# Performance work log

Hardware: AMD Instinct MI355X
Metric: run time of the kernel (lower is better)

## Reference

```python
import jax, jax.numpy as jnp
import numpy as np

EPS = 1e-7
BLOCK = 64  # block_size from init_kwargs


def project(x):
    norm = jnp.clip(jnp.linalg.norm(x, axis=-1, keepdims=True), EPS)
    return jnp.where(norm >= 1.0, x / norm * (1.0 - EPS), x)


def mobius_add(x, y, c):
    x2 = jnp.sum(x * x, -1, keepdims=True)
    y2 = jnp.sum(y * y, -1, keepdims=True)
    xy = jnp.sum(x * y, -1, keepdims=True)
    num = (1 + 2 * c * xy + c * y2) * x + (1 - c * x2) * y
    den = 1 + 2 * c * xy + c * c * x2 * y2
    return project(num / jnp.clip(den, EPS))


def logmap0(y, c):
    sqrt_c = jnp.clip(jnp.sqrt(c), EPS)
    yn = jnp.linalg.norm(y, axis=-1, keepdims=True)
    mag = jnp.arctanh(jnp.minimum(yn, 1.0 - EPS)) / sqrt_c
    return jnp.where(yn < EPS, jnp.zeros_like(y), mag * (y / jnp.clip(yn, EPS)))


def expmap0(v, c):
    sqrt_c = jnp.clip(jnp.sqrt(c), EPS)
    vn = jnp.linalg.norm(v, axis=-1, keepdims=True)
    mag = jnp.tanh(sqrt_c * jnp.clip(vn, EPS)) / sqrt_c
    return project(jnp.where(vn < EPS, jnp.zeros_like(v), mag * (v / jnp.clip(vn, EPS))))


def pdist(x, y, c):
    # x: [B,H,S,1,D], y: [B,H,1,S,D], c: [1,H,1,1,1] -> [B,H,S,S]
    sqrt_c = jnp.clip(jnp.sqrt(c), EPS)
    add_norm = jnp.linalg.norm(mobius_add(-x, y, c), axis=-1)
    sc = jnp.squeeze(sqrt_c, -1)
    arg = jnp.minimum(sc * add_norm, 1.0 - EPS)
    return 2.0 * jnp.arctanh(arg) / sc


def layernorm(x, scale, bias, eps=1e-6):
    mu = jnp.mean(x, -1, keepdims=True)
    var = jnp.mean(jnp.square(x - mu), -1, keepdims=True)
    return (x - mu) * jax.lax.rsqrt(var + eps) * scale + bias


def precompute_freqs_cis(dim, end, theta=10000.0):
    f = 1.0 / theta ** (jnp.arange(0, dim, 2, dtype=jnp.float32) / dim)
    return jnp.exp(1j * jnp.outer(jnp.arange(end), f))


def rope(x, fc):
    # split-half rotary, as in WubuBlock.apply_rotary_emb
    xr, xi = jnp.split(x, 2, -1)
    xc = jax.lax.complex(xr, xi) * fc.reshape(1, 1, fc.shape[0], fc.shape[1])
    return jnp.concatenate([xc.real, xc.imag], -1)


def setup_inputs() -> dict:
    key = jax.random.key(0)
    ks = jax.random.split(key, 8)
    B, N, D, H = 1, 1024, 512, 8
    w = lambda k, shape, s=0.02: jax.random.normal(k, shape, jnp.float32) * s
    return {
        'x': w(ks[0], (B, N, D), 0.02),  # points well inside the Poincare ball
        'c_global': jax.random.uniform(ks[1], (B, 1), jnp.float32, 0.5, 1.5),
        'W_qkv': w(ks[2], (D, 3 * D)), 'b_qkv': jnp.zeros((3 * D,), jnp.float32),
        'W_out': w(ks[3], (D, D)), 'b_out': jnp.zeros((D,), jnp.float32),
        'ln1_scale': jnp.ones((D,), jnp.float32), 'ln1_bias': jnp.zeros((D,), jnp.float32),
        'ln2_scale': jnp.ones((D,), jnp.float32), 'ln2_bias': jnp.zeros((D,), jnp.float32),
        'W_ff1': w(ks[4], (D, 4 * D)), 'b_ff1': jnp.zeros((4 * D,), jnp.float32),
        'W_ff2': w(ks[5], (4 * D, D)), 'b_ff2': jnp.zeros((D,), jnp.float32),
        'c_per_head_logits': jnp.zeros((H,), jnp.float32),
        'geo_scale': jnp.ones((1, H, 1, 1), jnp.float32),
        'start_pos': 0,
    }


def reference(x, c_global, W_qkv, b_qkv, W_out, b_out, ln1_scale, ln1_bias,
              ln2_scale, ln2_bias, W_ff1, b_ff1, W_ff2, b_ff2,
              c_per_head_logits, geo_scale, start_pos):
    B, N, D = x.shape
    H = c_per_head_logits.shape[0]
    hd = D // H
    S = BLOCK
    nb = N // S
    Be = B * nb
    xb = x.reshape(Be, S, D)
    c_b = jnp.repeat(c_global, nb, axis=0).reshape(Be, 1, 1)

    # tangent-space layernorm (norm1) then logmap to tangent for QKV proj
    xn = expmap0(layernorm(logmap0(xb, c_b), ln1_scale, ln1_bias), c_b)
    xt = logmap0(xn, c_b)
    qkv = (xt @ W_qkv + b_qkv).reshape(Be, S, 3, H, hd).transpose(2, 0, 3, 1, 4)
    q, k, v = qkv[0], qkv[1], qkv[2]  # [Be,H,S,hd]

    fc = precompute_freqs_cis(hd, S)
    q = rope(q, fc)
    k = rope(k, fc)

    c_h = jax.nn.softplus(c_per_head_logits).reshape(1, H, 1, 1)
    qh = expmap0(q, c_h)
    kh = expmap0(k, c_h)

    # full pairwise hyperbolic distance: [Be,H,S,S]
    d = pdist(qh[:, :, :, None, :], kh[:, :, None, :, :], c_h[:, :, None, :, :])
    attn = jax.nn.softmax(-geo_scale * d, axis=-1)
    ao = jnp.einsum('bhqk,bhkd->bhqd', attn, v)
    ao = ao.transpose(0, 2, 1, 3).reshape(Be, S, D)

    ah = expmap0(ao @ W_out + b_out, c_b)
    xa = mobius_add(xb, ah, c_b)  # hyperbolic residual

    # hyperbolic FFN with tangent-space norm (norm2)
    xn2 = expmap0(layernorm(logmap0(xa, c_b), ln2_scale, ln2_bias), c_b)
    t = logmap0(xn2, c_b)
    fh = expmap0(jax.nn.gelu(t @ W_ff1 + b_ff1) @ W_ff2 + b_ff2, c_b)
    out = mobius_add(xa, fh, c_b)
    return out.reshape(B, N, D)
```

## Files before the change

### kernel.cpp

```cpp
#include <hip/hip_runtime.h>
#include <math.h>

#define DEV __device__ __forceinline__
typedef _Float16 h16;
typedef __attribute__((ext_vector_type(8))) _Float16 h8v;
typedef __attribute__((ext_vector_type(4))) _Float16 h4v;
typedef __attribute__((ext_vector_type(4))) float f4v;

constexpr int NTOK = 1024;
constexpr int D    = 512;
constexpr int H    = 8;
constexpr int NB   = 16;
constexpr double EPSd = 1e-7;

DEV double wave_sum(double v) {
#pragma unroll
  for (int m = 32; m; m >>= 1) v += __shfl_xor(v, m, 64);
  return v;
}

__global__ void k_prep(const float* __restrict__ Wqkv, const float* __restrict__ Wout,
                       const float* __restrict__ Wff1, const float* __restrict__ Wff2,
                       const float* __restrict__ x, const float* __restrict__ cg,
                       const float* __restrict__ s1, const float* __restrict__ b1,
                       h16* __restrict__ qT, h16* __restrict__ oT,
                       h16* __restrict__ f1T, h16* __restrict__ f2T,
                       h16* __restrict__ xt) {
  __shared__ float t[32][33];
  const int bid = blockIdx.x;
  if (bid < 3072) {
    const float* src; h16* dh; int K, N, bx, by;
    if (bid < 768)       { src = Wqkv; dh = qT;  K = 512;  N = 1536; bx = bid % 48;          by = bid / 48; }
    else if (bid < 1024) { src = Wout; dh = oT;  K = 512;  N = 512;  bx = (bid - 768) % 16;  by = (bid - 768) / 16; }
    else if (bid < 2048) { src = Wff1; dh = f1T; K = 512;  N = 2048; bx = (bid - 1024) % 64; by = (bid - 1024) / 64; }
    else                 { src = Wff2; dh = f2T; K = 2048; N = 512;  bx = (bid - 2048) % 16; by = (bid - 2048) / 16; }
    const int n0 = bx * 32, k0 = by * 32;
    const int tx = threadIdx.x & 31, ty = threadIdx.x >> 5;
    for (int i = ty; i < 32; i += 8) t[i][tx] = src[(size_t)(k0 + i) * N + n0 + tx];
    __syncthreads();
    for (int i = ty; i < 32; i += 8)
      dh[(size_t)(n0 + i) * K + k0 + tx] = (h16)t[tx][i];
    return;
  }
  const int wid = threadIdx.x >> 6, lane = threadIdx.x & 63;
  const int tok = (bid - 3072) * 4 + wid;
  const float4* xr = (const float4*)(x + (size_t)tok * D);
  float4 xv0 = xr[lane], xv1 = xr[lane + 64];
  double sv = 0.0, svv = 0.0;
  {
    const float e[8] = {xv0.x, xv0.y, xv0.z, xv0.w, xv1.x, xv1.y, xv1.z, xv1.w};
#pragma unroll
    for (int j = 0; j < 8; ++j) { double d = e[j]; sv += d; svv += d * d; }
  }
  sv = wave_sum(sv); svv = wave_sum(svv);
  double c = (double)cg[0];
  double sc = sqrt(c); if (sc < EPSd) sc = EPSd;
  double yn = sqrt(svv);
  double arg0 = yn; if (arg0 > 1.0 - EPSd) arg0 = 1.0 - EPSd;
  double f = (yn < EPSd) ? 0.0 : atanh(arg0) / sc / fmax(yn, EPSd);
  double mu = f * sv / D;
  double var = f * f * svv / D - mu * mu;
  double rs = 1.0 / sqrt(var + 1e-6);
  const float4* s1r = (const float4*)s1;
  const float4* b1r = (const float4*)b1;
  float4 sA = s1r[lane], sB = s1r[lane + 64];
  float4 bA = b1r[lane], bB = b1r[lane + 64];
  double w[8]; double sww = 0.0;
  {
    const float e[8]  = {xv0.x, xv0.y, xv0.z, xv0.w, xv1.x, xv1.y, xv1.z, xv1.w};
    const float se[8] = {sA.x, sA.y, sA.z, sA.w, sB.x, sB.y, sB.z, sB.w};
    const float be[8] = {bA.x, bA.y, bA.z, bA.w, bB.x, bB.y, bB.z, bB.w};
#pragma unroll
    for (int j = 0; j < 8; ++j) {
      w[j] = (f * (double)e[j] - mu) * rs * (double)se[j] + (double)be[j];
      sww += w[j] * w[j];
    }
  }
  sww = wave_sum(sww);
  double vn = sqrt(sww);
  double F = 0.0;
  if (vn >= EPSd) {
    double mag_e = tanh(sc * fmax(vn, EPSd)) / sc;
    F = atanh(fmin(mag_e, 1.0 - EPSd)) / (sc * vn);
  }
  h16* dst = xt + (size_t)tok * D;
#pragma unroll
  for (int half = 0; half < 2; ++half) {
    h4v o;
#pragma unroll
    for (int e = 0; e < 4; ++e) o[e] = (h16)(float)(F * w[half * 4 + e]);
    *(h4v*)(dst + 4 * (lane + 64 * half)) = o;
  }
}

DEV void stage_tile(const h16* __restrict__ gbase, int rowstride, h16* lds,
                    int wid, int lane) {
#pragma unroll
  for (int j = 0; j < 2; ++j) {
    const int rbase = wid * 16 + j * 8;
    const int grow = rbase + (lane >> 3);
    const int gch = (lane & 7) ^ (lane >> 3);
    const h16* gp = gbase + (size_t)grow * rowstride + gch * 8;
    __builtin_amdgcn_global_load_lds(
        (const __attribute__((address_space(1))) void*)gp,
        (__attribute__((address_space(3))) void*)(lds + rbase * 64), 16, 0, 0);
  }
}
DEV h8v read_frag(const h16* lds, int row, int c) {
  const int p = c ^ (row & 7);
  return *(const h8v*)(lds + row * 64 + p * 8);
}

template <int GELU, int OHALF, int SPLITK>
__global__ __launch_bounds__(256) void k_mm(
    const h16* __restrict__ A, const h16* __restrict__ B,
    const float* __restrict__ bias, float* __restrict__ Cf, h16* __restrict__ Ch,
    int M, int N, int K) {
  __shared__ __align__(16) h16 As[2][64 * 64];
  __shared__ __align__(16) h16 Bs[2][64 * 64];
  const int tid = threadIdx.x;
  const int lane = tid & 63, wid = tid >> 6;
  const int wr = (wid >> 1) * 32, wc = (wid & 1) * 32;
  const int lr = lane & 15, lg = lane >> 4;
  const size_t r0 = (size_t)blockIdx.y * 64, c0 = (size_t)blockIdx.x * 64;
  const int kz = SPLITK ? blockIdx.z : 0;
  const int Keff = SPLITK ? (K >> 1) : K;
  const f4v z = {0.f, 0.f, 0.f, 0.f};
  f4v acc[2][2]; acc[0][0] = z; acc[0][1] = z; acc[1][0] = z; acc[1][1] = z;
  const h16* Abase = A + r0 * K + (size_t)kz * Keff;
  const h16* Bbase = B + c0 * K + (size_t)kz * Keff;
  const int NT = Keff >> 6;
  stage_tile(Abase, K, As[0], wid, lane);
  stage_tile(Bbase, K, Bs[0], wid, lane);
  int cur = 0;
  for (int t = 0; t < NT; ++t) {
    const int nxt = cur ^ 1;
    if (t + 1 < NT) {
      stage_tile(Abase + (t + 1) * 64, K, As[nxt], wid, lane);
      stage_tile(Bbase + (t + 1) * 64, K, Bs[nxt], wid, lane);
      asm volatile("s_waitcnt vmcnt(4)" ::: "memory");
    } else {
      asm volatile("s_waitcnt vmcnt(0)" ::: "memory");
    }
    asm volatile("s_barrier" ::: "memory");
    const h16* Ac = As[cur];
    const h16* Bc = Bs[cur];
#pragma unroll
    for (int ks = 0; ks < 2; ++ks) {
      const int c = ks * 4 + lg;
      h8v a0 = read_frag(Ac, wr + lr, c);
      h8v a1 = read_frag(Ac, wr + 16 + lr, c);
      h8v b0 = read_frag(Bc, wc + lr, c);
      h8v b1 = read_frag(Bc, wc + 16 + lr, c);
      acc[0][0] = __builtin_amdgcn_mfma_f32_16x16x32_f16(a0, b0, acc[0][0], 0, 0, 0);
      acc[0][1] = __builtin_amdgcn_mfma_f32_16x16x32_f16(a0, b1, acc[0][1], 0, 0, 0);
      acc[1][0] = __builtin_amdgcn_mfma_f32_16x16x32_f16(a1, b0, acc[1][0], 0, 0, 0);
      acc[1][1] = __builtin_amdgcn_mfma_f32_16x16x32_f16(a1, b1, acc[1][1], 0, 0, 0);
    }
    asm volatile("s_barrier" ::: "memory");
    cur = nxt;
  }
  float* Cfo = Cf + (size_t)kz * M * N;
#pragma unroll
  for (int m = 0; m < 2; ++m)
#pragma unroll
    for (int n = 0; n < 2; ++n) {
      const size_t row = r0 + wr + m * 16 + lg * 4;
      const size_t col = c0 + wc + n * 16 + lr;
      const float bv = (SPLITK && kz) ? 0.f : bias[col];
#pragma unroll
      for (int e = 0; e < 4; ++e) {
        float v = acc[m][n][e] + bv;
        if (GELU) {
          float x3 = v * v * v;
          v = 0.5f * v * (1.0f + tanhf(0.7978845608028654f * (v + 0.044715f * x3)));
        }
        if (OHALF) Ch[(row + e) * N + col] = (h16)v;
        else       Cfo[(row + e) * N + col] = v;
      }
    }
}

__global__ __launch_bounds__(256) void k_attn(
    const h16* __restrict__ qkv, const float* __restrict__ chl,
    const float* __restrict__ geo, h16* __restrict__ ao) {
  __shared__ __align__(16) float Qs[32][68];
  __shared__ __align__(16) float Kt[64][68];
  __shared__ __align__(16) float Vs[64][68];
  __shared__ float q2s[32], k2s[64], fqv[32], fkv[64];
  const int bid = blockIdx.x;
  const int be = bid >> 4, h = (bid >> 1) & 7, q0 = (bid & 1) * 32;
  const int tid = threadIdx.x;
  const double chd = log1p(exp((double)chl[h]));
  const float ch = (float)chd;
  float sc = (float)sqrt(chd); if (sc < 1e-7f) sc = 1e-7f;
  for (int l = tid; l < 64 * 32; l += 256) {
    int s = l >> 5, j = l & 31;
    const h16* base = qkv + (size_t)(be * 64 + s) * 1536 + h * 64;
    float ka = (float)base[512 + j], kb = (float)base[512 + j + 32];
    float fj = expf((float)j * -0.2878231366242557f);
    float st, ct; sincosf((float)s * fj, &st, &ct);
    Kt[j][s]      = ka * ct - kb * st;
    Kt[j + 32][s] = ka * st + kb * ct;
    Vs[s][j]      = (float)base[1024 + j];
    Vs[s][j + 32] = (float)base[1024 + j + 32];
  }
  for (int l = tid; l < 32 * 32; l += 256) {
    int s = l >> 5, j = l & 31;
    const h16* base = qkv + (size_t)(be * 64 + q0 + s) * 1536 + h * 64;
    float qa = (float)base[j], qb = (float)base[j + 32];
    float fj = expf((float)j * -0.2878231366242557f);
    float st, ct; sincosf((float)(q0 + s) * fj, &st, &ct);
    Qs[s][j]      = qa * ct - qb * st;
    Qs[s][j + 32] = qa * st + qb * ct;
  }
  __syncthreads();
  if (tid < 64) {
    float a = 0.f;
    for (int d2 = 0; d2 < 64; ++d2) { float v = Kt[d2][tid]; a += v * v; }
    float n = sqrtf(a);
    float m = tanhf(sc * fmaxf(n, 1e-7f)) / sc;
    float f = (n < 1e-7f) ? 0.f : m / fmaxf(n, 1e-7f);
    if (m >= 1.f) f *= (1.f - 1e-7f) / m;
    float fn = f * n;
    fkv[tid] = f; k2s[tid] = fn * fn;
  } else if (tid < 96) {
    int i = tid - 64;
    float a = 0.f;
    for (int d2 = 0; d2 < 64; ++d2) { float v = Qs[i][d2]; a += v * v; }
    float n = sqrtf(a);
    float m = tanhf(sc * fmaxf(n, 1e-7f)) / sc;
    float f = (n < 1e-7f) ? 0.f : m / fmaxf(n, 1e-7f);
    if (m >= 1.f) f *= (1.f - 1e-7f) / m;
    float fn = f * n;
    fqv[i] = f; q2s[i] = fn * fn;
  }
  __syncthreads();
  const int i = tid >> 3, g = tid & 7;
  float gacc[8];
#pragma unroll
  for (int jj = 0; jj < 8; ++jj) gacc[jj] = 0.f;
  for (int d2 = 0; d2 < 64; ++d2) {
    float qv = Qs[i][d2];
    const float4* kp = (const float4*)&Kt[d2][g * 8];
    float4 k0 = kp[0], k1 = kp[1];
    gacc[0] += qv * k0.x; gacc[1] += qv * k0.y; gacc[2] += qv * k0.z; gacc[3] += qv * k0.w;
    gacc[4] += qv * k1.x; gacc[5] += qv * k1.y; gacc[6] += qv * k1.z; gacc[7] += qv * k1.w;
  }
  const float gs = geo[h];
  const float q2 = q2s[i], fqi = fqv[i];
  float lg[8];
  float mx = -1e30f;
#pragma unroll
  for (int jj = 0; jj < 8; ++jj) {
    float gq = fqi * fkv[g * 8 + jj] * gacc[jj];
    float k2 = k2s[g * 8 + jj];
    float A  = 1.f - 2.f * ch * gq + ch * k2;
    float Bv = 1.f - ch * q2;
    float n2 = fmaxf(A * A * q2 - 2.f * A * Bv * gq + Bv * Bv * k2, 0.f);
    float den = fmaxf(1.f - 2.f * ch * gq + ch * ch * q2 * k2, 1e-7f);
    float r = fminf(sqrtf(n2) / den, 1.f - 1e-7f);
    float arg = fminf(sc * r, 1.f - 1e-7f);
    float l = -gs * (2.f * atanhf(arg) / sc);
    lg[jj] = l; mx = fmaxf(mx, l);
  }
  mx = fmaxf(mx, __shfl_xor(mx, 1, 64));
  mx = fmaxf(mx, __shfl_xor(mx, 2, 64));
  mx = fmaxf(mx, __shfl_xor(mx, 4, 64));
  float pv[8]; float sum = 0.f;
#pragma unroll
  for (int jj = 0; jj < 8; ++jj) { pv[jj] = expf(lg[jj] - mx); sum += pv[jj]; }
  sum += __shfl_xor(sum, 1, 64);
  sum += __shfl_xor(sum, 2, 64);
  sum += __shfl_xor(sum, 4, 64);
  float inv = 1.0f / sum;
#pragma unroll
  for (int jj = 0; jj < 8; ++jj) Qs[i][g * 8 + jj] = pv[jj] * inv;
  float oacc[8];
#pragma unroll
  for (int dd = 0; dd < 8; ++dd) oacc[dd] = 0.f;
  for (int jv = 0; jv < 64; ++jv) {
    float p = Qs[i][jv];
    const float4* vp = (const float4*)&Vs[jv][g * 8];
    float4 v0 = vp[0], v1 = vp[1];
    oacc[0] += p * v0.x; oacc[1] += p * v0.y; oacc[2] += p * v0.z; oacc[3] += p * v0.w;
    oacc[4] += p * v1.x; oacc[5] += p * v1.y; oacc[6] += p * v1.z; oacc[7] += p * v1.w;
  }
#pragma unroll
  for (int dd = 0; dd < 8; ++dd)
    ao[(size_t)(be * 64 + q0 + i) * D + h * 64 + g * 8 + dd] = (h16)oacc[dd];
}

__global__ void k_resid(const float* __restrict__ x, const float* __restrict__ proj,
                        const float* __restrict__ cg, const float* __restrict__ s2,
                        const float* __restrict__ b2, float* __restrict__ xa,
                        h16* __restrict__ t2) {
  const int wid = threadIdx.x >> 6, lane = threadIdx.x & 63;
  const int tok = blockIdx.x * 4 + wid;
  const float4* xr  = (const float4*)(x + (size_t)tok * D);
  const float4* p0r = (const float4*)(proj + (size_t)tok * D);
  const float4* p1r = (const float4*)(proj + (size_t)NTOK * D + (size_t)tok * D);
  float4 xv0 = xr[lane], xv1 = xr[lane + 64];
  float4 pa0 = p0r[lane], pa1 = p0r[lane + 64];
  float4 pb0 = p1r[lane], pb1 = p1r[lane + 64];
  float pe[8], xe[8];
  xe[0]=xv0.x; xe[1]=xv0.y; xe[2]=xv0.z; xe[3]=xv0.w; xe[4]=xv1.x; xe[5]=xv1.y; xe[6]=xv1.z; xe[7]=xv1.w;
  pe[0]=pa0.x+pb0.x; pe[1]=pa0.y+pb0.y; pe[2]=pa0.z+pb0.z; pe[3]=pa0.w+pb0.w;
  pe[4]=pa1.x+pb1.x; pe[5]=pa1.y+pb1.y; pe[6]=pa1.z+pb1.z; pe[7]=pa1.w+pb1.w;
  double sx = 0, sp = 0, xx = 0, pp = 0, xp = 0;
#pragma unroll
  for (int j = 0; j < 8; ++j) {
    double dx = xe[j], dp = pe[j];
    sx += dx; sp += dp; xx += dx * dx; pp += dp * dp; xp += dx * dp;
  }
  sx = wave_sum(sx); sp = wave_sum(sp); xx = wave_sum(xx);
  pp = wave_sum(pp); xp = wave_sum(xp);
  double c = (double)cg[0];
  double sc = sqrt(c); if (sc < EPSd) sc = EPSd;
  double pn = sqrt(pp);
  double me = tanh(sc * fmax(pn, EPSd)) / sc;
  double fs = (pn < EPSd) ? 0.0 : me / fmax(pn, EPSd);
  if (me >= 1.0) fs *= (1.0 - EPSd) / me;
  double y2 = fs * fs * pp, xy = fs * xp;
  double a = 1.0 + 2.0 * c * xy + c * y2;
  double b = 1.0 - c * xx;
  double den = 1.0 + 2.0 * c * xy + c * c * xx * y2;
  if (den < EPSd) den = EPSd;
  double zn = sqrt(fmax(a * a * xx + 2.0 * a * b * xy + b * b * y2, 0.0)) / den;
  double zs = 1.0 / den;
  if (zn >= 1.0) zs *= (1.0 - EPSd) / zn;
  double xan = (zn >= 1.0) ? (1.0 - EPSd) : zn;
  double A0 = zs * a, B0 = zs * b * fs;
  double xav[8];
#pragma unroll
  for (int j = 0; j < 8; ++j) xav[j] = A0 * (double)xe[j] + B0 * (double)pe[j];
  {
    float4 o0 = {(float)xav[0], (float)xav[1], (float)xav[2], (float)xav[3]};
    float4 o1 = {(float)xav[4], (float)xav[5], (float)xav[6], (float)xav[7]};
    float4* xw = (float4*)(xa + (size_t)tok * D);
    xw[lane] = o0; xw[lane + 64] = o1;
  }
  double sxa  = A0 * sx + B0 * sp;
  double sxa2 = A0 * A0 * xx + 2.0 * A0 * B0 * xp + B0 * B0 * pp;
  double fl = 0.0;
  if (xan >= EPSd) fl = atanh(fmin(xan, 1.0 - EPSd)) / (sc * fmax(xan, EPSd));
  double mu = fl * sxa / D;
  double var = fl * fl * sxa2 / D - mu * mu;
  double rs = 1.0 / sqrt(var + 1e-6);
  const float4* s2r = (const float4*)s2;
  const float4* b2r = (const float4*)b2;
  float4 sA = s2r[lane], sB = s2r[lane + 64];
  float4 bA = b2r[lane], bB = b2r[lane + 64];
  const float se[8] = {sA.x, sA.y, sA.z, sA.w, sB.x, sB.y, sB.z, sB.w};
  const float be[8] = {bA.x, bA.y, bA.z, bA.w, bB.x, bB.y, bB.z, bB.w};
  double w[8]; double sww = 0.0;
#pragma unroll
  for (int j = 0; j < 8; ++j) {
    w[j] = (fl * xav[j] - mu) * rs * (double)se[j] + (double)be[j];
    sww += w[j] * w[j];
  }
  sww = wave_sum(sww);
  double vn = sqrt(sww);
  double F = 0.0;
  if (vn >= EPSd) {
    double mag_e = tanh(sc * fmax(vn, EPSd)) / sc;
    F = atanh(fmin(mag_e, 1.0 - EPSd)) / (sc * vn);
  }
  h16* dst = t2 + (size_t)tok * D;
#pragma unroll
  for (int half = 0; half < 2; ++half) {
    h4v o;
#pragma unroll
    for (int e = 0; e < 4; ++e) o[e] = (h16)(float)(F * w[half * 4 + e]);
    *(h4v*)(dst + 4 * (lane + 64 * half)) = o;
  }
}

__global__ void k_final(const float* __restrict__ xa, const float* __restrict__ f2,
                        const float* __restrict__ cg, float* __restrict__ out) {
  const int wid = threadIdx.x >> 6, lane = threadIdx.x & 63;
  const int tok = blockIdx.x * 4 + wid;
  const float4* ar  = (const float4*)(xa + (size_t)tok * D);
  const float4* f0r = (const float4*)(f2 + (size_t)tok * D);
  const float4* f1r = (const float4*)(f2 + (size_t)NTOK * D + (size_t)tok * D);
  float4 xv0 = ar[lane], xv1 = ar[lane + 64];
  float4 pa0 = f0r[lane], pa1 = f0r[lane + 64];
  float4 pb0 = f1r[lane], pb1 = f1r[lane + 64];
  float pe[8], xe[8];
  xe[0]=xv0.x; xe[1]=xv0.y; xe[2]=xv0.z; xe[3]=xv0.w; xe[4]=xv1.x; xe[5]=xv1.y; xe[6]=xv1.z; xe[7]=xv1.w;
  pe[0]=pa0.x+pb0.x; pe[1]=pa0.y+pb0.y; pe[2]=pa0.z+pb0.z; pe[3]=pa0.w+pb0.w;
  pe[4]=pa1.x+pb1.x; pe[5]=pa1.y+pb1.y; pe[6]=pa1.z+pb1.z; pe[7]=pa1.w+pb1.w;
  double xx = 0, pp = 0, xp = 0;
#pragma unroll
  for (int j = 0; j < 8; ++j) {
    double dx = xe[j], dp = pe[j];
    xx += dx * dx; pp += dp * dp; xp += dx * dp;
  }
  xx = wave_sum(xx); pp = wave_sum(pp); xp = wave_sum(xp);
  double c = (double)cg[0];
  double sc = sqrt(c); if (sc < EPSd) sc = EPSd;
  double pn = sqrt(pp);
  double me = tanh(sc * fmax(pn, EPSd)) / sc;
  double fs = (pn < EPSd) ? 0.0 : me / fmax(pn, EPSd);
  if (me >= 1.0) fs *= (1.0 - EPSd) / me;
  double y2 = fs * fs * pp, xy = fs * xp;
  double a = 1.0 + 2.0 * c * xy + c * y2;
  double b = 1.0 - c * xx;
  double den = 1.0 + 2.0 * c * xy + c * c * xx * y2;
  if (den < EPSd) den = EPSd;
  double zn = sqrt(fmax(a * a * xx + 2.0 * a * b * xy + b * b * y2, 0.0)) / den;
  double zs = 1.0 / den;
  if (zn >= 1.0) zs *= (1.0 - EPSd) / zn;
  double A0 = zs * a, B0 = zs * b * fs;
  float4 o0, o1;
  o0.x = (float)(A0 * xe[0] + B0 * pe[0]); o0.y = (float)(A0 * xe[1] + B0 * pe[1]);
  o0.z = (float)(A0 * xe[2] + B0 * pe[2]); o0.w = (float)(A0 * xe[3] + B0 * pe[3]);
  o1.x = (float)(A0 * xe[4] + B0 * pe[4]); o1.y = (float)(A0 * xe[5] + B0 * pe[5]);
  o1.z = (float)(A0 * xe[6] + B0 * pe[6]); o1.w = (float)(A0 * xe[7] + B0 * pe[7]);
  float4* ow = (float4*)(out + (size_t)tok * D);
  ow[lane] = o0; ow[lane + 64] = o1;
}

extern "C" void kernel_launch(void* const* d_in, const int* in_sizes, int n_in,
                              void* d_out, int out_size, void* d_ws, size_t ws_size,
                              hipStream_t stream) {
  (void)in_sizes; (void)n_in; (void)out_size; (void)ws_size;
  const float* x    = (const float*)d_in[0];
  const float* cg   = (const float*)d_in[1];
  const float* Wqkv = (const float*)d_in[2];
  const float* bqkv = (const float*)d_in[3];
  const float* Wout = (const float*)d_in[4];
  const float* bout = (const float*)d_in[5];
  const float* s1   = (const float*)d_in[6];
  const float* b1   = (const float*)d_in[7];
  const float* s2   = (const float*)d_in[8];
  const float* b2   = (const float*)d_in[9];
  const float* Wff1 = (const float*)d_in[10];
  const float* bff1 = (const float*)d_in[11];
  const float* Wff2 = (const float*)d_in[12];
  const float* bff2 = (const float*)d_in[13];
  const float* chl  = (const float*)d_in[14];
  const float* geo  = (const float*)d_in[15];
  float* out = (float*)d_out;

  char* base = (char*)d_ws;
  const size_t MB = 1024 * 1024;
  h16*   WqkvT = (h16*)(base + 0);
  h16*   WoutT = (h16*)(base + (3*MB)/2);
  h16*   Wff1T = (h16*)(base + 2*MB);
  h16*   Wff2T = (h16*)(base + 4*MB);
  h16*   xt    = (h16*)(base + 6*MB);
  h16*   qkv   = (h16*)(base + 7*MB);
  h16*   ao    = (h16*)(base + 10*MB);
  float* proj  = (float*)(base + 11*MB);
  float* xa    = (float*)(base + 7*MB);
  h16*   t2    = (h16*)(base + 6*MB);
  h16*   h1    = (h16*)(base + 11*MB);
  float* f2    = (float*)(base + 0);

  k_prep<<<3072 + NTOK / 4, 256, 0, stream>>>(Wqkv, Wout, Wff1, Wff2, x, cg, s1, b1,
                                              WqkvT, WoutT, Wff1T, Wff2T, xt);
  k_mm<0, 1, 0><<<dim3(1536 / 64, NTOK / 64), 256, 0, stream>>>(
      xt, WqkvT, bqkv, nullptr, qkv, NTOK, 1536, 512);
  k_attn<<<NB * H * 2, 256, 0, stream>>>(qkv, chl, geo, ao);
  k_mm<0, 0, 1><<<dim3(512 / 64, NTOK / 64, 2), 256, 0, stream>>>(
      ao, WoutT, bout, proj, nullptr, NTOK, 512, 512);
  k_resid<<<NTOK / 4, 256, 0, stream>>>(x, proj, cg, s2, b2, xa, t2);
  k_mm<1, 1, 0><<<dim3(2048 / 64, NTOK / 64), 256, 0, stream>>>(
      t2, Wff1T, bff1, nullptr, h1, NTOK, 2048, 512);
  k_mm<0, 0, 1><<<dim3(512 / 64, NTOK / 64, 2), 256, 0, stream>>>(
      h1, Wff2T, bff2, f2, nullptr, NTOK, 512, 2048);
  k_final<<<NTOK / 4, 256, 0, stream>>>(xa, f2, cg, out);
}
```

Before: 74.89 us.

## Triple-buffer GEMM tiles and vectorize attention Q/K/V staging with fused norms

The GEMM kernel moves from a double-buffered to a triple-buffered LDS pipeline, prefetching two K-tiles ahead with adjusted vmcnt waits so global loads overlap more MFMA work. The attention kernel loads Q, K and V with 16-byte half8 vector loads, one thread per 8-element chunk, and computes the squared norms during RoPE using the rotation-invariance of the norm. This removes the serial 64-step LDS norm loops, and the output store becomes a single 16-byte write. The costs are 50% more LDS per GEMM block, which can lower occupancy, and more live registers in the staging loop.

```diff
diff --git a/kernel.cpp b/kernel.cpp
--- a/kernel.cpp
+++ b/kernel.cpp
@@ -116,8 +116,8 @@
     const h16* __restrict__ A, const h16* __restrict__ B,
     const float* __restrict__ bias, float* __restrict__ Cf, h16* __restrict__ Ch,
     int M, int N, int K) {
-  __shared__ __align__(16) h16 As[2][64 * 64];
-  __shared__ __align__(16) h16 Bs[2][64 * 64];
+  __shared__ __align__(16) h16 As[3][64 * 64];
+  __shared__ __align__(16) h16 Bs[3][64 * 64];
   const int tid = threadIdx.x;
   const int lane = tid & 63, wid = tid >> 6;
   const int wr = (wid >> 1) * 32, wc = (wid & 1) * 32;
@@ -132,16 +132,20 @@
   const int NT = Keff >> 6;
   stage_tile(Abase, K, As[0], wid, lane);
   stage_tile(Bbase, K, Bs[0], wid, lane);
+  stage_tile(Abase + 64, K, As[1], wid, lane);
+  stage_tile(Bbase + 64, K, Bs[1], wid, lane);
   int cur = 0;
   for (int t = 0; t < NT; ++t) {
-    const int nxt = cur ^ 1;
-    if (t + 1 < NT) {
-      stage_tile(Abase + (t + 1) * 64, K, As[nxt], wid, lane);
-      stage_tile(Bbase + (t + 1) * 64, K, Bs[nxt], wid, lane);
-      asm volatile("s_waitcnt vmcnt(4)" ::: "memory");
-    } else {
-      asm volatile("s_waitcnt vmcnt(0)" ::: "memory");
+    const int pre = (cur == 2) ? 0 : cur + 1;
+    const int pre2 = (pre == 2) ? 0 : pre + 1;
+    if (t + 2 < NT) {
+      stage_tile(Abase + (t + 2) * 64, K, As[pre2], wid, lane);
+      stage_tile(Bbase + (t + 2) * 64, K, Bs[pre2], wid, lane);
     }
+    const int rem = NT - 1 - t;
+    if (rem >= 2)      asm volatile("s_waitcnt vmcnt(8)" ::: "memory");
+    else if (rem == 1) asm volatile("s_waitcnt vmcnt(4)" ::: "memory");
+    else               asm volatile("s_waitcnt vmcnt(0)" ::: "memory");
     asm volatile("s_barrier" ::: "memory");
     const h16* Ac = As[cur];
     const h16* Bc = Bs[cur];
@@ -158,7 +162,7 @@
       acc[1][1] = __builtin_amdgcn_mfma_f32_16x16x32_f16(a1, b1, acc[1][1], 0, 0, 0);
     }
     asm volatile("s_barrier" ::: "memory");
-    cur = nxt;
+    cur = pre;
   }
   float* Cfo = Cf + (size_t)kz * M * N;
 #pragma unroll
@@ -187,6 +191,7 @@
   __shared__ __align__(16) float Qs[32][68];
   __shared__ __align__(16) float Kt[64][68];
   __shared__ __align__(16) float Vs[64][68];
+  __shared__ float q2raw[32], k2raw[64];
   __shared__ float q2s[32], k2s[64], fqv[32], fkv[64];
   const int bid = blockIdx.x;
   const int be = bid >> 4, h = (bid >> 1) & 7, q0 = (bid & 1) * 32;
@@ -194,31 +199,61 @@
   const double chd = log1p(exp((double)chl[h]));
   const float ch = (float)chd;
   float sc = (float)sqrt(chd); if (sc < 1e-7f) sc = 1e-7f;
-  for (int l = tid; l < 64 * 32; l += 256) {
-    int s = l >> 5, j = l & 31;
+  {
+    const int s = tid >> 2, jc = (tid & 3) * 8;
     const h16* base = qkv + (size_t)(be * 64 + s) * 1536 + h * 64;
-    float ka = (float)base[512 + j], kb = (float)base[512 + j + 32];
-    float fj = expf((float)j * -0.2878231366242557f);
-    float st, ct; sincosf((float)s * fj, &st, &ct);
-    Kt[j][s]      = ka * ct - kb * st;
-    Kt[j + 32][s] = ka * st + kb * ct;
-    Vs[s][j]      = (float)base[1024 + j];
-    Vs[s][j + 32] = (float)base[1024 + j + 32];
-  }
-  for (int l = tid; l < 32 * 32; l += 256) {
-    int s = l >> 5, j = l & 31;
+    h8v klo = *(const h8v*)(base + 512 + jc);
+    h8v khi = *(const h8v*)(base + 512 + jc + 32);
+    h8v vlo = *(const h8v*)(base + 1024 + jc);
+    h8v vhi = *(const h8v*)(base + 1024 + jc + 32);
+    float racc = 0.f;
+#pragma unroll
+    for (int j = 0; j < 8; ++j) {
+      float ka = (float)klo[j], kb = (float)khi[j];
+      racc += ka * ka + kb * kb;
+      float fj = expf((float)(jc + j) * -0.2878231366242557f);
+      float st, ct; sincosf((float)s * fj, &st, &ct);
+      Kt[jc + j][s]      = ka * ct - kb * st;
+      Kt[jc + j + 32][s] = ka * st + kb * ct;
+    }
+    float4 v0, v1;
+#pragma unroll
+    for (int j = 0; j < 4; ++j) { v0[j] = (float)vlo[j]; v1[j] = (float)vlo[j + 4]; }
+    *(float4*)&Vs[s][jc] = v0; *(float4*)&Vs[s][jc + 4] = v1;
+#pragma unroll
+    for (int j = 0; j < 4; ++j) { v0[j] = (float)vhi[j]; v1[j] = (float)vhi[j + 4]; }
+    *(float4*)&Vs[s][jc + 32] = v0; *(float4*)&Vs[s][jc + 36] = v1;
+    racc += __shfl_xor(racc, 1, 64);
+    racc += __shfl_xor(racc, 2, 64);
+    if ((tid & 3) == 0) k2raw[s] = racc;
+  }
+  if (tid < 128) {
+    const int s = tid >> 2, jc = (tid & 3) * 8;
     const h16* base = qkv + (size_t)(be * 64 + q0 + s) * 1536 + h * 64;
-    float qa = (float)base[j], qb = (float)base[j + 32];
-    float fj = expf((float)j * -0.2878231366242557f);
-    float st, ct; sincosf((float)(q0 + s) * fj, &st, &ct);
-    Qs[s][j]      = qa * ct - qb * st;
-    Qs[s][j + 32] = qa * st + qb * ct;
+    h8v qlo = *(const h8v*)(base + jc);
+    h8v qhi = *(const h8v*)(base + jc + 32);
+    float racc = 0.f;
+    float rl[8], rh[8];
+#pragma unroll
+    for (int j = 0; j < 8; ++j) {
+      float qa = (float)qlo[j], qb = (float)qhi[j];
+      racc += qa * qa + qb * qb;
+      float fj = expf((float)(jc + j) * -0.2878231366242557f);
+      float st, ct; sincosf((float)(q0 + s) * fj, &st, &ct);
+      rl[j] = qa * ct - qb * st;
+      rh[j] = qa * st + qb * ct;
+    }
+    *(float4*)&Qs[s][jc]      = {rl[0], rl[1], rl[2], rl[3]};
+    *(float4*)&Qs[s][jc + 4]  = {rl[4], rl[5], rl[6], rl[7]};
+    *(float4*)&Qs[s][jc + 32] = {rh[0], rh[1], rh[2], rh[3]};
+    *(float4*)&Qs[s][jc + 36] = {rh[4], rh[5], rh[6], rh[7]};
+    racc += __shfl_xor(racc, 1, 64);
+    racc += __shfl_xor(racc, 2, 64);
+    if ((tid & 3) == 0) q2raw[s] = racc;
   }
   __syncthreads();
   if (tid < 64) {
-    float a = 0.f;
-    for (int d2 = 0; d2 < 64; ++d2) { float v = Kt[d2][tid]; a += v * v; }
-    float n = sqrtf(a);
+    float n = sqrtf(k2raw[tid]);
     float m = tanhf(sc * fmaxf(n, 1e-7f)) / sc;
     float f = (n < 1e-7f) ? 0.f : m / fmaxf(n, 1e-7f);
     if (m >= 1.f) f *= (1.f - 1e-7f) / m;
@@ -226,9 +261,7 @@
     fkv[tid] = f; k2s[tid] = fn * fn;
   } else if (tid < 96) {
     int i = tid - 64;
-    float a = 0.f;
-    for (int d2 = 0; d2 < 64; ++d2) { float v = Qs[i][d2]; a += v * v; }
-    float n = sqrtf(a);
+    float n = sqrtf(q2raw[i]);
     float m = tanhf(sc * fmaxf(n, 1e-7f)) / sc;
     float f = (n < 1e-7f) ? 0.f : m / fmaxf(n, 1e-7f);
     if (m >= 1.f) f *= (1.f - 1e-7f) / m;
@@ -286,9 +319,10 @@
     oacc[0] += p * v0.x; oacc[1] += p * v0.y; oacc[2] += p * v0.z; oacc[3] += p * v0.w;
     oacc[4] += p * v1.x; oacc[5] += p * v1.y; oacc[6] += p * v1.z; oacc[7] += p * v1.w;
   }
-#pragma unroll
-  for (int dd = 0; dd < 8; ++dd)
-    ao[(size_t)(be * 64 + q0 + i) * D + h * 64 + g * 8 + dd] = (h16)oacc[dd];
+  h8v ov;
+#pragma unroll
+  for (int dd = 0; dd < 8; ++dd) ov[dd] = (h16)oacc[dd];
+  *(h8v*)(ao + (size_t)(be * 64 + q0 + i) * D + h * 64 + g * 8) = ov;
 }
 
 __global__ void k_resid(const float* __restrict__ x, const float* __restrict__ proj,
```

New measurement: 73.41 us. 2.0% less time.
